# Performance work log

Measured on AMD Instinct MI355X. Metric: run time of the kernel, lower is better.

The kernel has to match this reference:

```python
import jax, jax.numpy as jnp
import numpy as np


def setup_inputs() -> dict:
    key = jax.random.key(0)
    ks = jax.random.split(key, 10)
    B, S, H, I, V = 64, 2048, 512, 512, 50257
    scale = 0.05
    return {
        "last_output": jax.random.randint(ks[0], (B,), 0, V),
        "last_hidden": jax.random.normal(ks[1], (1, B, H), jnp.float32),
        "encoder_outputs": jax.random.normal(ks[2], (S, B, H), jnp.float32),
        "embedding": jax.random.normal(ks[3], (V, I), jnp.float32) * scale,
        "W_ih": jax.random.normal(ks[4], (3 * H, I + H), jnp.float32) * scale,
        "b_ih": jax.random.normal(ks[5], (3 * H,), jnp.float32) * scale,
        "W_hh": jax.random.normal(ks[6], (3 * H, H), jnp.float32) * scale,
        "b_hh": jax.random.normal(ks[7], (3 * H,), jnp.float32) * scale,
        "W_out": jax.random.normal(ks[8], (V, 2 * H), jnp.float32) * scale,
        "b_out": jax.random.normal(ks[9], (V,), jnp.float32) * scale,
    }


def _gru_step(x, h, W_ih, b_ih, W_hh, b_hh):
    # torch nn.GRU parametrization, single layer, single timestep.
    H = h.shape[-1]
    gi = x @ W_ih.T + b_ih  # [B, 3H]
    gh = h @ W_hh.T + b_hh  # [B, 3H]
    i_r, i_z, i_n = gi[:, :H], gi[:, H:2 * H], gi[:, 2 * H:]
    h_r, h_z, h_n = gh[:, :H], gh[:, H:2 * H], gh[:, 2 * H:]
    r = jax.nn.sigmoid(i_r + h_r)
    z = jax.nn.sigmoid(i_z + h_z)
    n = jnp.tanh(i_n + r * h_n)
    return (1.0 - z) * n + z * h


def reference(last_output, last_hidden, encoder_outputs, embedding,
              W_ih, b_ih, W_hh, b_hh, W_out, b_out):
    # Embedding lookup: [B, I]
    embedded = embedding[last_output]
    h_top = last_hidden[-1]  # [B, H]
    # Luong 'dot' attention: score(b, s) = h_b . enc[s, b]
    scores = jnp.einsum('bh,sbh->bs', h_top, encoder_outputs)  # [B, S]
    attn = jax.nn.softmax(scores, axis=-1)                      # [B, S]
    # context = attn @ enc (per batch): [B, H]
    context = jnp.einsum('bs,sbh->bh', attn, encoder_outputs)
    # GRU single step on cat(embedded, context)
    rnn_in = jnp.concatenate([embedded, context], axis=-1)      # [B, I+H]
    h_new = _gru_step(rnn_in, h_top, W_ih, b_ih, W_hh, b_hh)    # [B, H]
    # Output projection on cat(rnn_out, context) -> log_softmax over vocab
    feat = jnp.concatenate([h_new, context], axis=-1)           # [B, 2H]
    logits = feat @ W_out.T + b_out                             # [B, V]
    logp = jax.nn.log_softmax(logits, axis=-1)
    hidden = h_new[None]  # [1, B, H]
    return logp, hidden
```

## Files before the change

kernel.cpp:

```cpp
#include <hip/hip_runtime.h>
#include <hip/hip_bf16.h>
#include <math.h>

#define BB 64
#define SS 2048
#define HH 512
#define VV 50257
#define KD 1024
#define NSPLIT 32
#define NTILE 786

typedef float f32x4 __attribute__((ext_vector_type(4)));
typedef __bf16 bf16x8 __attribute__((ext_vector_type(8)));

__device__ __forceinline__ float dot4(float4 a, float4 b) {
  return a.x*b.x + a.y*b.y + a.z*b.z + a.w*b.w;
}

__device__ __forceinline__ bf16x8 cvt8(float4 a, float4 b) {
  bf16x8 r;
  r[0]=(__bf16)a.x; r[1]=(__bf16)a.y; r[2]=(__bf16)a.z; r[3]=(__bf16)a.w;
  r[4]=(__bf16)b.x; r[5]=(__bf16)b.y; r[6]=(__bf16)b.z; r[7]=(__bf16)b.w;
  return r;
}

__device__ __forceinline__ size_t fragAddr(int b, int k) {
  return (size_t)(k >> 5)*2048 + (size_t)(b >> 4)*512
       + (size_t)((k >> 3) & 3)*128 + (size_t)(b & 15)*8 + (size_t)(k & 7);
}

__global__ __launch_bounds__(256) void attn_partial(
    const float* __restrict__ hprev, const float* __restrict__ enc,
    float* __restrict__ pm, float* __restrict__ pl, float* __restrict__ pacc)
{
  const int b = blockIdx.x >> 5;
  const int split = blockIdx.x & 31;
  const int t = threadIdx.x;
  const int w = t >> 6, lane = t & 63;

  const float* hb = hprev + b*HH + lane*8;
  const float4 h0 = *(const float4*)hb;
  const float4 h1 = *(const float4*)(hb + 4);
  const int s0 = split*64 + w*16;

  float m = -INFINITY, lsum = 0.f;
  float acc[8];
#pragma unroll
  for (int j = 0; j < 8; ++j) acc[j] = 0.f;

#pragma unroll 1
  for (int half = 0; half < 2; ++half) {
    float4 ea[8], eb[8];
#pragma unroll
    for (int i = 0; i < 8; ++i) {
      const float* ep = enc + ((size_t)(s0 + half*8 + i)*BB + b)*HH + lane*8;
      ea[i] = *(const float4*)ep; eb[i] = *(const float4*)(ep + 4);
    }
    float dd[8];
#pragma unroll
    for (int i = 0; i < 8; ++i) dd[i] = dot4(h0, ea[i]) + dot4(h1, eb[i]);
#pragma unroll
    for (int off = 32; off >= 1; off >>= 1) {
#pragma unroll
      for (int i = 0; i < 8; ++i) dd[i] += __shfl_xor(dd[i], off, 64);
    }
    float hm = dd[0];
#pragma unroll
    for (int i = 1; i < 8; ++i) hm = fmaxf(hm, dd[i]);
    const float mn = fmaxf(m, hm);
    const float sc = __expf(m - mn);
    float p[8], psum = 0.f;
#pragma unroll
    for (int i = 0; i < 8; ++i) { p[i] = __expf(dd[i] - mn); psum += p[i]; }
    lsum = lsum*sc + psum;
#pragma unroll
    for (int j = 0; j < 8; ++j) acc[j] *= sc;
#pragma unroll
    for (int i = 0; i < 8; ++i) {
      acc[0] += p[i]*ea[i].x; acc[1] += p[i]*ea[i].y;
      acc[2] += p[i]*ea[i].z; acc[3] += p[i]*ea[i].w;
      acc[4] += p[i]*eb[i].x; acc[5] += p[i]*eb[i].y;
      acc[6] += p[i]*eb[i].z; acc[7] += p[i]*eb[i].w;
    }
    m = mn;
  }

  __shared__ float sm4[4], sl4[4];
  __shared__ float sacc[4][HH];
  if (lane == 0) { sm4[w] = m; sl4[w] = lsum; }
  __syncthreads();
  const float M = fmaxf(fmaxf(sm4[0], sm4[1]), fmaxf(sm4[2], sm4[3]));
  const float ew = __expf(m - M);
#pragma unroll
  for (int j = 0; j < 8; ++j) sacc[w][lane*8 + j] = acc[j]*ew;
  __syncthreads();

  const int rec = blockIdx.x;
  for (int hh = t; hh < HH; hh += 256)
    pacc[(size_t)rec*HH + hh] = sacc[0][hh]+sacc[1][hh]+sacc[2][hh]+sacc[3][hh];
  if (t == 0) {
    float L = sl4[0]*__expf(sm4[0]-M) + sl4[1]*__expf(sm4[1]-M)
            + sl4[2]*__expf(sm4[2]-M) + sl4[3]*__expf(sm4[3]-M);
    pm[rec] = M; pl[rec] = L;
  }
}

__global__ __launch_bounds__(256) void attn_reduce(
    const float* __restrict__ pm, const float* __restrict__ pl,
    const float* __restrict__ pacc, __hip_bfloat16* __restrict__ featA)
{
  const int b = blockIdx.x, t = threadIdx.x;
  __shared__ float smm[NSPLIT], sll[NSPLIT], sco[NSPLIT];
  if (t < NSPLIT) { smm[t] = pm[b*NSPLIT + t]; sll[t] = pl[b*NSPLIT + t]; }
  __syncthreads();
  float M = -INFINITY;
  for (int q = 0; q < NSPLIT; ++q) M = fmaxf(M, smm[q]);
  float L = 0.f;
  for (int q = 0; q < NSPLIT; ++q) L += sll[q]*__expf(smm[q]-M);
  const float inv = 1.f/L;
  if (t < NSPLIT) sco[t] = __expf(smm[t]-M)*inv;
  __syncthreads();
  const int hh0 = 2*t;
  float s0 = 0.f, s1 = 0.f;
  for (int q = 0; q < NSPLIT; ++q) {
    const float* pq = pacc + ((size_t)b*NSPLIT + q)*HH;
    s0 += pq[hh0]   * sco[q];
    s1 += pq[hh0+1] * sco[q];
  }
  const size_t a = fragAddr(b, HH + hh0);
  featA[a]   = (__hip_bfloat16)s0;
  featA[a+1] = (__hip_bfloat16)s1;
}

__global__ __launch_bounds__(256) void gru_gemm(
    const int* __restrict__ last_out, const float* __restrict__ emb,
    const float* __restrict__ hprev, const __hip_bfloat16* __restrict__ featA,
    const float* __restrict__ W_ih, const float* __restrict__ W_hh,
    float* __restrict__ gates)
{
  const int u = blockIdx.x;
  const int gt = u / 12;
  const int rem = u % 12;
  const int seg = rem >> 2, ks = rem & 3;
  const int w = threadIdx.x >> 6, lane = threadIdx.x & 63;
  const int col = lane & 15, kg = lane >> 4;
  const int g = gt*64 + w*16 + col;

  const float* wrow = (seg == 2) ? (W_hh + (size_t)g*HH)
                                 : (W_ih + (size_t)g*KD + seg*HH);
  int lo_r[4];
#pragma unroll
  for (int mt = 0; mt < 4; ++mt) lo_r[mt] = last_out[mt*16 + col];

  f32x4 acc[4];
#pragma unroll
  for (int mt = 0; mt < 4; ++mt) acc[mt] = (f32x4){0.f,0.f,0.f,0.f};

  const int kbeg = ks*128, kend = kbeg + 128;
  for (int k0 = kbeg; k0 < kend; k0 += 32) {
    const float* wp = wrow + k0 + kg*8;
    const bf16x8 bf = cvt8(*(const float4*)wp, *(const float4*)(wp+4));
#pragma unroll
    for (int mt = 0; mt < 4; ++mt) {
      const int bb = mt*16 + col;
      bf16x8 af;
      if (seg == 0) {
        const float* ap = emb + (size_t)lo_r[mt]*HH + k0 + kg*8;
        af = cvt8(*(const float4*)ap, *(const float4*)(ap+4));
      } else if (seg == 1) {
        af = *(const bf16x8*)(featA + fragAddr(bb, HH + k0 + kg*8));
      } else {
        const float* ap = hprev + (size_t)bb*HH + k0 + kg*8;
        af = cvt8(*(const float4*)ap, *(const float4*)(ap+4));
      }
      acc[mt] = __builtin_amdgcn_mfma_f32_16x16x32_bf16(af, bf, acc[mt], 0, 0, 0);
    }
  }

  float* gp = gates + (size_t)rem*BB*1536;
#pragma unroll
  for (int mt = 0; mt < 4; ++mt)
#pragma unroll
    for (int reg = 0; reg < 4; ++reg) {
      const int brow = mt*16 + kg*4 + reg;
      gp[(size_t)brow*1536 + g] = acc[mt][reg];
    }
}

__global__ __launch_bounds__(512) void gru_pointwise(
    const float* __restrict__ gates, const float* __restrict__ hprev,
    const float* __restrict__ b_ih, const float* __restrict__ b_hh,
    float* __restrict__ hid_out, __hip_bfloat16* __restrict__ featA)
{
  const int b = blockIdx.x, j = threadIdx.x;

  float i_r = 0.f, i_z = 0.f, i_n = 0.f;
#pragma unroll
  for (int p = 0; p < 8; ++p) {
    const float* gp = gates + ((size_t)p*BB + b)*1536;
    i_r += gp[j]; i_z += gp[HH + j]; i_n += gp[2*HH + j];
  }
  float h_r = 0.f, h_z = 0.f, h_n = 0.f;
#pragma unroll
  for (int p = 8; p < 12; ++p) {
    const float* gp = gates + ((size_t)p*BB + b)*1536;
    h_r += gp[j]; h_z += gp[HH + j]; h_n += gp[2*HH + j];
  }

  const float r = 1.f/(1.f + __expf(-(i_r + h_r + b_ih[j] + b_hh[j])));
  const float z = 1.f/(1.f + __expf(-(i_z + h_z + b_ih[HH+j] + b_hh[HH+j])));
  const float n = tanhf(i_n + b_ih[2*HH+j] + r*(h_n + b_hh[2*HH+j]));
  const float hp = hprev[b*HH + j];
  const float hn = (1.f - z)*n + z*hp;
  hid_out[b*HH + j] = hn;
  featA[fragAddr(b, j)] = (__hip_bfloat16)hn;
}

__global__ __launch_bounds__(256) void logits_gemm(
    const __hip_bfloat16* __restrict__ featA, const float* __restrict__ W_out,
    const float* __restrict__ b_out, float* __restrict__ out,
    float* __restrict__ pmE, float* __restrict__ plE)
{
  __shared__ float vals[64*65];
  __shared__ float pMq[4*64], pLq[4*64];
  const int tile = blockIdx.x;
  const int t = threadIdx.x;
  const int w = t >> 6, lane = t & 63;
  const int col = lane & 15, kg = lane >> 4;
  const int v = tile*64 + w*16 + col;
  const int vc = (v < VV) ? v : (VV - 1);

  const float* wp = W_out + (size_t)vc*KD + kg*8;
  const __hip_bfloat16* fp = featA + lane*8;

  f32x4 acc[4];
#pragma unroll
  for (int mt = 0; mt < 4; ++mt) acc[mt] = (f32x4){0.f,0.f,0.f,0.f};

  float4 WA[3], WB[3];
  bf16x8 AF[3][4];

#pragma unroll
  for (int s = 0; s < 2; ++s) {
    WA[s] = *(const float4*)(wp + s*32);
    WB[s] = *(const float4*)(wp + s*32 + 4);
    const __hip_bfloat16* f = fp + s*2048;
    AF[s][0] = *(const bf16x8*)(f);
    AF[s][1] = *(const bf16x8*)(f + 512);
    AF[s][2] = *(const bf16x8*)(f + 1024);
    AF[s][3] = *(const bf16x8*)(f + 1536);
  }

#pragma unroll
  for (int kc = 0; kc < 32; ++kc) {
    if (kc + 2 < 32) {
      const int s = (kc + 2) % 3;
      WA[s] = *(const float4*)(wp + (kc+2)*32);
      WB[s] = *(const float4*)(wp + (kc+2)*32 + 4);
      const __hip_bfloat16* f = fp + (kc+2)*2048;
      AF[s][0] = *(const bf16x8*)(f);
      AF[s][1] = *(const bf16x8*)(f + 512);
      AF[s][2] = *(const bf16x8*)(f + 1024);
      AF[s][3] = *(const bf16x8*)(f + 1536);
    }
    const int c = kc % 3;
    const bf16x8 bf = cvt8(WA[c], WB[c]);
    acc[0] = __builtin_amdgcn_mfma_f32_16x16x32_bf16(AF[c][0], bf, acc[0], 0, 0, 0);
    acc[1] = __builtin_amdgcn_mfma_f32_16x16x32_bf16(AF[c][1], bf, acc[1], 0, 0, 0);
    acc[2] = __builtin_amdgcn_mfma_f32_16x16x32_bf16(AF[c][2], bf, acc[2], 0, 0, 0);
    acc[3] = __builtin_amdgcn_mfma_f32_16x16x32_bf16(AF[c][3], bf, acc[3], 0, 0, 0);
  }

  const float bo = (v < VV) ? b_out[v] : 0.f;
#pragma unroll
  for (int mt = 0; mt < 4; ++mt)
#pragma unroll
    for (int reg = 0; reg < 4; ++reg) {
      const float val = acc[mt][reg] + bo;
      const int brow = mt*16 + kg*4 + reg;
      if (v < VV) out[(size_t)brow*VV + v] = val;
      vals[brow*65 + w*16 + col] = (v < VV) ? val : -INFINITY;
    }
  __syncthreads();

  {
    const int row = t & 63, q = t >> 6;
    const float* vr = vals + row*65 + q*16;
    float M = -INFINITY;
#pragma unroll
    for (int i = 0; i < 16; ++i) M = fmaxf(M, vr[i]);
    float L = 0.f;
    if (M > -INFINITY) {
#pragma unroll
      for (int i = 0; i < 16; ++i) L += __expf(vr[i] - M);
    }
    pMq[q*64 + row] = M; pLq[q*64 + row] = L;
  }
  __syncthreads();
  if (t < 64) {
    float M = pMq[t], L = pLq[t];
#pragma unroll
    for (int q = 1; q < 4; ++q) {
      const float mq = pMq[q*64 + t], lq = pLq[q*64 + t];
      if (mq > -INFINITY) {
        const float mn = fmaxf(M, mq);
        L = L*__expf(M - mn) + lq*__expf(mq - mn);
        M = mn;
      }
    }
    pmE[t*1024 + tile] = M; plE[t*1024 + tile] = L;
  }
}

__global__ __launch_bounds__(256) void lsm_rowreduce(
    const float* __restrict__ pmE, const float* __restrict__ plE,
    float* __restrict__ cvec)
{
  const int t = threadIdx.x;
  const int w = t >> 6, lane = t & 63;
  const int row = blockIdx.x*4 + w;
  if (row >= BB) return;
  float M = -INFINITY, L = 0.f;
  for (int q = lane; q < NTILE; q += 64) {
    const float mq = pmE[row*1024 + q], lq = plE[row*1024 + q];
    const float mn = fmaxf(M, mq);
    L = L*__expf(M - mn) + lq*__expf(mq - mn);
    M = mn;
  }
#pragma unroll
  for (int off = 32; off >= 1; off >>= 1) {
    const float m2 = __shfl_xor(M, off, 64), l2 = __shfl_xor(L, off, 64);
    const float mn = fmaxf(M, m2);
    L = L*__expf(M - mn) + l2*__expf(m2 - mn);
    M = mn;
  }
  if (lane == 0) cvec[row] = M + logf(L);
}

__global__ __launch_bounds__(256) void lsm_sub(
    float* __restrict__ out, const float* __restrict__ cvec)
{
  const unsigned total4 = (unsigned)(BB*(unsigned)VV/4u);
  const unsigned idx = blockIdx.x*256u + threadIdx.x;
  if (idx >= total4) return;
  const unsigned i = idx*4u;
  float4 v = *(float4*)(out + i);
  v.x -= cvec[i/VV];
  v.y -= cvec[(i+1)/VV];
  v.z -= cvec[(i+2)/VV];
  v.w -= cvec[(i+3)/VV];
  *(float4*)(out + i) = v;
}

extern "C" void kernel_launch(void* const* d_in, const int* in_sizes, int n_in,
                              void* d_out, int out_size, void* d_ws, size_t ws_size,
                              hipStream_t stream)
{
  const int*   last_output = (const int*)d_in[0];
  const float* last_hidden = (const float*)d_in[1];
  const float* enc         = (const float*)d_in[2];
  const float* emb         = (const float*)d_in[3];
  const float* W_ih        = (const float*)d_in[4];
  const float* b_ih        = (const float*)d_in[5];
  const float* W_hh        = (const float*)d_in[6];
  const float* b_hh        = (const float*)d_in[7];
  const float* W_out       = (const float*)d_in[8];
  const float* b_out       = (const float*)d_in[9];
  float* out = (float*)d_out;

  __hip_bfloat16* featA = (__hip_bfloat16*)d_ws;
  float* gates = (float*)((char*)d_ws + 131072);
  float* pm   = gates + (size_t)12*BB*1536;
  float* pl   = pm + BB*NSPLIT;
  float* pmE  = pl + BB*NSPLIT;
  float* plE  = pmE + BB*1024;
  float* cvec = plE + BB*1024;
  float* pacc = out;
  float* hid_out = out + (size_t)BB*VV;

  attn_partial <<<dim3(BB*NSPLIT), dim3(256), 0, stream>>>(last_hidden, enc, pm, pl, pacc);
  attn_reduce  <<<dim3(BB),        dim3(256), 0, stream>>>(pm, pl, pacc, featA);
  gru_gemm     <<<dim3(24*12),     dim3(256), 0, stream>>>(last_output, emb, last_hidden,
                                                           featA, W_ih, W_hh, gates);
  gru_pointwise<<<dim3(BB),        dim3(512), 0, stream>>>(gates, last_hidden, b_ih, b_hh,
                                                           hid_out, featA);
  logits_gemm  <<<dim3(NTILE),     dim3(256), 0, stream>>>(featA, W_out, b_out, out, pmE, plE);
  lsm_rowreduce<<<dim3(16),        dim3(256), 0, stream>>>(pmE, plE, cvec);
  lsm_sub      <<<dim3((int)(((size_t)BB*VV/4 + 255)/256)), dim3(256), 0, stream>>>(out, cvec);
}
```

Baseline: 165.3 us.

## Fuse log-softmax row reduction into subtraction kernel and deepen logits prefetch

Removes the separate lsm_rowreduce launch. Each lsm_sub block now recomputes the log-sum-exp for the one or two rows its 1024-element chunk spans, reading the per-tile max and sum partials directly. It also raises the W_out and feature prefetch depth in logits_gemm from two stages ahead to three, using bitmask indexing. In exchange, many blocks redundantly reduce the same 786 partials per row, and the extra prefetch buffers raise register pressure.

```diff
diff --git a/kernel.cpp b/kernel.cpp
--- a/kernel.cpp
+++ b/kernel.cpp
@@ -237,11 +237,11 @@
 #pragma unroll
   for (int mt = 0; mt < 4; ++mt) acc[mt] = (f32x4){0.f,0.f,0.f,0.f};
 
-  float4 WA[3], WB[3];
-  bf16x8 AF[3][4];
-
-#pragma unroll
-  for (int s = 0; s < 2; ++s) {
+  float4 WA[4], WB[4];
+  bf16x8 AF[4][4];
+
+#pragma unroll
+  for (int s = 0; s < 3; ++s) {
     WA[s] = *(const float4*)(wp + s*32);
     WB[s] = *(const float4*)(wp + s*32 + 4);
     const __hip_bfloat16* f = fp + s*2048;
@@ -253,17 +253,17 @@
 
 #pragma unroll
   for (int kc = 0; kc < 32; ++kc) {
-    if (kc + 2 < 32) {
-      const int s = (kc + 2) % 3;
-      WA[s] = *(const float4*)(wp + (kc+2)*32);
-      WB[s] = *(const float4*)(wp + (kc+2)*32 + 4);
-      const __hip_bfloat16* f = fp + (kc+2)*2048;
+    if (kc + 3 < 32) {
+      const int s = (kc + 3) & 3;
+      WA[s] = *(const float4*)(wp + (kc+3)*32);
+      WB[s] = *(const float4*)(wp + (kc+3)*32 + 4);
+      const __hip_bfloat16* f = fp + (kc+3)*2048;
       AF[s][0] = *(const bf16x8*)(f);
       AF[s][1] = *(const bf16x8*)(f + 512);
       AF[s][2] = *(const bf16x8*)(f + 1024);
       AF[s][3] = *(const bf16x8*)(f + 1536);
     }
-    const int c = kc % 3;
+    const int c = kc & 3;
     const bf16x8 bf = cvt8(WA[c], WB[c]);
     acc[0] = __builtin_amdgcn_mfma_f32_16x16x32_bf16(AF[c][0], bf, acc[0], 0, 0, 0);
     acc[1] = __builtin_amdgcn_mfma_f32_16x16x32_bf16(AF[c][1], bf, acc[1], 0, 0, 0);
@@ -312,43 +312,49 @@
   }
 }
 
-__global__ __launch_bounds__(256) void lsm_rowreduce(
-    const float* __restrict__ pmE, const float* __restrict__ plE,
-    float* __restrict__ cvec)
+__global__ __launch_bounds__(256) void lsm_sub(
+    float* __restrict__ out, const float* __restrict__ pmE,
+    const float* __restrict__ plE)
 {
   const int t = threadIdx.x;
-  const int w = t >> 6, lane = t & 63;
-  const int row = blockIdx.x*4 + w;
-  if (row >= BB) return;
-  float M = -INFINITY, L = 0.f;
-  for (int q = lane; q < NTILE; q += 64) {
-    const float mq = pmE[row*1024 + q], lq = plE[row*1024 + q];
-    const float mn = fmaxf(M, mq);
-    L = L*__expf(M - mn) + lq*__expf(mq - mn);
-    M = mn;
-  }
-#pragma unroll
-  for (int off = 32; off >= 1; off >>= 1) {
-    const float m2 = __shfl_xor(M, off, 64), l2 = __shfl_xor(L, off, 64);
-    const float mn = fmaxf(M, m2);
-    L = L*__expf(M - mn) + l2*__expf(m2 - mn);
-    M = mn;
-  }
-  if (lane == 0) cvec[row] = M + logf(L);
-}
-
-__global__ __launch_bounds__(256) void lsm_sub(
-    float* __restrict__ out, const float* __restrict__ cvec)
-{
-  const unsigned total4 = (unsigned)(BB*(unsigned)VV/4u);
-  const unsigned idx = blockIdx.x*256u + threadIdx.x;
-  if (idx >= total4) return;
-  const unsigned i = idx*4u;
+  const int wv = t >> 6, lane = t & 63;
+  const size_t off = (size_t)blockIdx.x * 1024;
+  const size_t total = (size_t)BB*VV;
+  __shared__ float cs[2];
+  __shared__ int rowA_s;
+
+  if (wv < 2) {
+    size_t pos = (wv == 0) ? off : (off + 1023 < total ? off + 1023 : total - 1);
+    const int row = (int)(pos / VV);
+    float M = -INFINITY, L = 0.f;
+    for (int q = lane; q < NTILE; q += 64) {
+      const float mq = pmE[row*1024 + q], lq = plE[row*1024 + q];
+      const float mn = fmaxf(M, mq);
+      L = L*__expf(M - mn) + lq*__expf(mq - mn);
+      M = mn;
+    }
+#pragma unroll
+    for (int o = 32; o >= 1; o >>= 1) {
+      const float m2 = __shfl_xor(M, o, 64), l2 = __shfl_xor(L, o, 64);
+      const float mn = fmaxf(M, m2);
+      L = L*__expf(M - mn) + l2*__expf(m2 - mn);
+      M = mn;
+    }
+    if (lane == 0) {
+      cs[wv] = M + logf(L);
+      if (wv == 0) rowA_s = row;
+    }
+  }
+  __syncthreads();
+
+  const size_t i = off + (size_t)t*4;
+  if (i >= total) return;
+  const size_t rs = (size_t)(rowA_s + 1)*VV;
   float4 v = *(float4*)(out + i);
-  v.x -= cvec[i/VV];
-  v.y -= cvec[(i+1)/VV];
-  v.z -= cvec[(i+2)/VV];
-  v.w -= cvec[(i+3)/VV];
+  v.x -= (i     >= rs) ? cs[1] : cs[0];
+  v.y -= (i + 1 >= rs) ? cs[1] : cs[0];
+  v.z -= (i + 2 >= rs) ? cs[1] : cs[0];
+  v.w -= (i + 3 >= rs) ? cs[1] : cs[0];
   *(float4*)(out + i) = v;
 }
 
@@ -374,7 +380,6 @@
   float* pl   = pm + BB*NSPLIT;
   float* pmE  = pl + BB*NSPLIT;
   float* plE  = pmE + BB*1024;
-  float* cvec = plE + BB*1024;
   float* pacc = out;
   float* hid_out = out + (size_t)BB*VV;
 
@@ -385,6 +390,5 @@
   gru_pointwise<<<dim3(BB),        dim3(512), 0, stream>>>(gates, last_hidden, b_ih, b_hh,
                                                            hid_out, featA);
   logits_gemm  <<<dim3(NTILE),     dim3(256), 0, stream>>>(featA, W_out, b_out, out, pmE, plE);
-  lsm_rowreduce<<<dim3(16),        dim3(256), 0, stream>>>(pmE, plE, cvec);
-  lsm_sub      <<<dim3((int)(((size_t)BB*VV/4 + 255)/256)), dim3(256), 0, stream>>>(out, cvec);
-}
+  lsm_sub      <<<dim3((int)(((size_t)BB*VV + 1023)/1024)), dim3(256), 0, stream>>>(out, pmE, plE);
+}
```

Measured after the change: 169.5 us. 1.03x slower.
